# Kernel optimization log

Hardware: AMD Instinct MI355X
Metric: run time of the kernel (lower is better)

Reference implementation:

```python
import jax, jax.numpy as jnp
import numpy as np

N_NODES = 50000


def setup_inputs() -> dict:
    key = jax.random.key(0)
    ks = jax.random.split(key, 6)
    d_in, d_out = 256, 256
    n_edges = 1_600_000
    x = jax.random.normal(ks[0], (N_NODES, d_in), dtype=jnp.float32)
    edge_index = jax.random.randint(ks[1], (2, n_edges), 0, N_NODES, dtype=jnp.int64)
    edge_attr = jax.random.normal(ks[2], (n_edges, 16), dtype=jnp.float32)  # unused by forward
    W1 = jax.random.normal(ks[3], (d_in, d_out), dtype=jnp.float32) * (1.0 / np.sqrt(d_in))
    b1 = jnp.zeros((d_out,), dtype=jnp.float32)
    W2 = jax.random.normal(ks[4], (d_out, d_out), dtype=jnp.float32) * (1.0 / np.sqrt(d_out))
    b2 = jnp.zeros((d_out,), dtype=jnp.float32)
    eps = jnp.zeros((1,), dtype=jnp.float32)  # train_eps=True, init 0
    return {"x": x, "edge_index": edge_index, "edge_attr": edge_attr,
            "W1": W1, "b1": b1, "W2": W2, "b2": b2, "eps": eps}


def reference(x, edge_index, edge_attr, W1, b1, W2, b2, eps):
    src, dst = edge_index[0], edge_index[1]
    # sum aggregation: agg[i] = sum_{(j->i) in E} x[j]
    agg = jax.ops.segment_sum(x[src], dst, num_segments=N_NODES)  # [N, d_in]
    h = (1.0 + eps[0]) * x + agg
    # MLP: Linear -> ReLU -> (dropout=0) -> Linear
    h = jax.nn.relu(h @ W1 + b1)
    out = h @ W2 + b2
    return out
```

## Files before the change

kernel.cpp:

```cpp
#include <hip/hip_runtime.h>
#include <stdint.h>

#define NODES 50000
#define D 256
#define MP 50048
#define NBUCK 196
#define CAP 10240
#define EPB 4096
#define HS_LD 264

typedef short bf16x8 __attribute__((ext_vector_type(8)));
typedef float f32x4 __attribute__((ext_vector_type(4)));

__device__ inline unsigned short f2b(float f) {
    unsigned int u = __float_as_uint(f);
    unsigned int r = (u + 0x7fffu + ((u >> 16) & 1u)) >> 16;
    return (unsigned short)r;
}

__device__ inline bool ei_is64(const int* ei) {
    return (ei[1] | ei[3] | ei[5] | ei[7]) == 0;
}
__device__ inline int ei_get(const int* __restrict__ ei, long long pos, bool is64) {
    return is64 ? ei[2 * pos] : ei[(int)pos];
}

__global__ __launch_bounds__(256) void cast_x_kernel(const float* __restrict__ x,
                                                     unsigned short* __restrict__ xb,
                                                     int* __restrict__ bcnt) {
    if (blockIdx.x == 0 && threadIdx.x < NBUCK) bcnt[threadIdx.x] = 0;
    int t = blockIdx.x * 256 + threadIdx.x;
    float4 v = ((const float4*)x)[t];
    unsigned int lo = (unsigned int)f2b(v.x) | ((unsigned int)f2b(v.y) << 16);
    unsigned int hi = (unsigned int)f2b(v.z) | ((unsigned int)f2b(v.w) << 16);
    ((uint2*)xb)[t] = make_uint2(lo, hi);
}

__global__ __launch_bounds__(256) void pack_w_kernel(const float* __restrict__ W1,
                                                     const float* __restrict__ W2,
                                                     unsigned short* __restrict__ P1,
                                                     unsigned short* __restrict__ P2) {
    int t = blockIdx.x * 256 + threadIdx.x;
    const float* W = (t < 8192) ? W1 : W2;
    unsigned short* P = (t < 8192) ? P1 : P2;
    int u = t & 8191;
    int lane = u & 63, nt = (u >> 6) & 15, s = u >> 10;
    int q = lane >> 4, n = nt * 16 + (lane & 15);
    int kbase = s * 32 + q * 8;
#pragma unroll
    for (int j = 0; j < 8; j++) P[u * 8 + j] = f2b(W[(kbase + j) * D + n]);
}

__global__ __launch_bounds__(256) void partA_kernel(const int* __restrict__ ei, int E,
                                                    int* __restrict__ bcnt,
                                                    unsigned int* __restrict__ ebufT) {
    __shared__ int cnt[256];
    __shared__ int gbase[256];
    __shared__ int lcur[256];
    bool is64 = ei_is64(ei);
    int tid = threadIdx.x;
    cnt[tid] = 0;
    lcur[tid] = 0;
    __syncthreads();
    long long blockStart = (long long)blockIdx.x * EPB;
    unsigned int w[16];
    int bk[16];
#pragma unroll
    for (int r = 0; r < 16; r++) {
        long long e = blockStart + r * 256 + tid;
        bk[r] = -1;
        if (e < E) {
            int src = ei_get(ei, e, is64);
            int dst = ei_get(ei, (long long)E + e, is64);
            bk[r] = dst >> 8;
            w[r] = ((unsigned int)(dst & 255) << 16) | (unsigned int)src;
            atomicAdd(&cnt[bk[r]], 1);
        }
    }
    __syncthreads();
    if (tid < NBUCK && cnt[tid] > 0) gbase[tid] = atomicAdd(&bcnt[tid], cnt[tid]);
    __syncthreads();
#pragma unroll
    for (int r = 0; r < 16; r++) {
        if (bk[r] >= 0) {
            int p = atomicAdd(&lcur[bk[r]], 1);
            ebufT[(size_t)bk[r] * CAP + gbase[bk[r]] + p] = w[r];
        }
    }
}

__global__ __launch_bounds__(256) void bscan_kernel(const int* __restrict__ bcnt,
                                                    int* __restrict__ bstart,
                                                    int* __restrict__ offs, int E) {
    __shared__ int buf[256];
    int tid = threadIdx.x;
    int v = (tid < NBUCK) ? bcnt[tid] : 0;
    buf[tid] = v;
    __syncthreads();
    for (int off = 1; off < 256; off <<= 1) {
        int xv = (tid >= off) ? buf[tid - off] : 0;
        __syncthreads();
        buf[tid] += xv;
        __syncthreads();
    }
    if (tid < NBUCK) bstart[tid] = buf[tid] - v;
    if (tid == 0) offs[NODES] = E;
}

__global__ __launch_bounds__(256) void partB_kernel(const int* __restrict__ bcnt,
                                                    const int* __restrict__ bstart,
                                                    const unsigned int* __restrict__ ebufT,
                                                    int* __restrict__ offs,
                                                    int* __restrict__ ebuf) {
    __shared__ int ncnt[256];
    __shared__ int ncur[256];
    int b = blockIdx.x, tid = threadIdx.x;
    int n = bcnt[b];
    int base = bstart[b];
    ncnt[tid] = 0;
    __syncthreads();
    const unsigned int* reg = ebufT + (size_t)b * CAP;
    for (int i = tid; i < n; i += 256) {
        unsigned int w = reg[i];
        atomicAdd(&ncnt[w >> 16], 1);
    }
    __syncthreads();
    int v = ncnt[tid];
    ncur[tid] = v;
    __syncthreads();
    for (int off = 1; off < 256; off <<= 1) {
        int xv = (tid >= off) ? ncur[tid - off] : 0;
        __syncthreads();
        ncur[tid] += xv;
        __syncthreads();
    }
    int excl = ncur[tid] - v;
    int node = b * 256 + tid;
    if (node < NODES) offs[node] = base + excl;
    __syncthreads();
    ncur[tid] = excl;
    __syncthreads();
    for (int i = tid; i < n; i += 256) {
        unsigned int w = reg[i];
        int p = atomicAdd(&ncur[w >> 16], 1);
        ebuf[base + p] = (int)(w & 0xffffu);
    }
}

__device__ inline void upk_add(uint4 w, float* a) {
    a[0] += __uint_as_float(w.x << 16);
    a[1] += __uint_as_float(w.x & 0xffff0000u);
    a[2] += __uint_as_float(w.y << 16);
    a[3] += __uint_as_float(w.y & 0xffff0000u);
    a[4] += __uint_as_float(w.z << 16);
    a[5] += __uint_as_float(w.z & 0xffff0000u);
    a[6] += __uint_as_float(w.w << 16);
    a[7] += __uint_as_float(w.w & 0xffff0000u);
}

__global__ __launch_bounds__(256) void agg_kernel(const unsigned short* __restrict__ xb,
                                                  const int* __restrict__ offs,
                                                  const int* __restrict__ ebuf,
                                                  const float* __restrict__ eps,
                                                  unsigned short* __restrict__ h0) {
    int wv = (blockIdx.x * 256 + threadIdx.x) >> 6;
    int lane = threadIdx.x & 63;
    if (wv >= NODES) return;
    int half = lane >> 5;
    int l32 = lane & 31;
    float aA[8] = {0, 0, 0, 0, 0, 0, 0, 0};
    float aB[8] = {0, 0, 0, 0, 0, 0, 0, 0};
    int beg = offs[wv], end = offs[wv + 1];
    for (int base = beg; base < end; base += 64) {
        int id = 0;
        if (base + lane < end) id = ebuf[base + lane];
        int m = min(64, end - base);
        int j = 0;
        for (; j + 4 <= m; j += 4) {
            int sA = __shfl(id, j + half);
            int sB = __shfl(id, j + 2 + half);
            uint4 wA = *(const uint4*)(xb + (size_t)sA * D + l32 * 8);
            uint4 wB = *(const uint4*)(xb + (size_t)sB * D + l32 * 8);
            upk_add(wA, aA);
            upk_add(wB, aB);
        }
        for (; j + 2 <= m; j += 2) {
            int sA = __shfl(id, j + half);
            uint4 wA = *(const uint4*)(xb + (size_t)sA * D + l32 * 8);
            upk_add(wA, aA);
        }
        if (j < m) {
            int sA = __shfl(id, j);
            if (half == 0) {
                uint4 wA = *(const uint4*)(xb + (size_t)sA * D + l32 * 8);
                upk_add(wA, aA);
            }
        }
    }
    float a[8];
#pragma unroll
    for (int i = 0; i < 8; i++) {
        a[i] = aA[i] + aB[i];
        a[i] += __shfl_xor(a[i], 32);
    }
    if (half == 0) {
        float scale = 1.0f + eps[0];
        uint4 v = *(const uint4*)(xb + (size_t)wv * D + l32 * 8);
        a[0] += scale * __uint_as_float(v.x << 16);
        a[1] += scale * __uint_as_float(v.x & 0xffff0000u);
        a[2] += scale * __uint_as_float(v.y << 16);
        a[3] += scale * __uint_as_float(v.y & 0xffff0000u);
        a[4] += scale * __uint_as_float(v.z << 16);
        a[5] += scale * __uint_as_float(v.z & 0xffff0000u);
        a[6] += scale * __uint_as_float(v.w << 16);
        a[7] += scale * __uint_as_float(v.w & 0xffff0000u);
        uint4 o;
        o.x = (unsigned int)f2b(a[0]) | ((unsigned int)f2b(a[1]) << 16);
        o.y = (unsigned int)f2b(a[2]) | ((unsigned int)f2b(a[3]) << 16);
        o.z = (unsigned int)f2b(a[4]) | ((unsigned int)f2b(a[5]) << 16);
        o.w = (unsigned int)f2b(a[6]) | ((unsigned int)f2b(a[7]) << 16);
        ((uint4*)(h0 + (size_t)wv * D))[l32] = o;
    }
}

__global__ __launch_bounds__(256) void gemm_fused_kernel(const unsigned short* __restrict__ A,
                                                         const unsigned short* __restrict__ P1,
                                                         const float* __restrict__ b1,
                                                         const unsigned short* __restrict__ P2,
                                                         const float* __restrict__ b2,
                                                         float* __restrict__ out, int Mvalid) {
    __shared__ unsigned short hs[64 * HS_LD];
    int wv = threadIdx.x >> 6;
    int lane = threadIdx.x & 63;
    int quad = lane >> 4, l16 = lane & 15;
    int mBase = blockIdx.x * 64;
    const bf16x8* B1v = (const bf16x8*)P1;
    const bf16x8* B2v = (const bf16x8*)P2;

    {
        f32x4 acc[4][4] = {};
#pragma unroll
        for (int ks = 0; ks < 8; ks++) {
            bf16x8 af[4], bf[4];
#pragma unroll
            for (int mi = 0; mi < 4; mi++) {
                int row = mBase + mi * 16 + l16;
                af[mi] = *(const bf16x8*)(A + (size_t)row * D + ks * 32 + quad * 8);
            }
#pragma unroll
            for (int ni = 0; ni < 4; ni++) bf[ni] = B1v[(ks * 16 + wv * 4 + ni) * 64 + lane];
#pragma unroll
            for (int mi = 0; mi < 4; mi++)
#pragma unroll
                for (int ni = 0; ni < 4; ni++)
                    acc[mi][ni] = __builtin_amdgcn_mfma_f32_16x16x32_bf16(af[mi], bf[ni],
                                                                          acc[mi][ni], 0, 0, 0);
        }
#pragma unroll
        for (int mi = 0; mi < 4; mi++)
#pragma unroll
            for (int ni = 0; ni < 4; ni++) {
                int col = wv * 64 + ni * 16 + l16;
                float bs = b1[col];
#pragma unroll
                for (int r = 0; r < 4; r++) {
                    int rl = mi * 16 + quad * 4 + r;
                    hs[rl * HS_LD + col] = f2b(fmaxf(acc[mi][ni][r] + bs, 0.0f));
                }
            }
    }
    __syncthreads();

    f32x4 acc[4][4] = {};
#pragma unroll
    for (int ks = 0; ks < 8; ks++) {
        bf16x8 af[4], bf[4];
#pragma unroll
        for (int mi = 0; mi < 4; mi++)
            af[mi] = *(const bf16x8*)(hs + (mi * 16 + l16) * HS_LD + ks * 32 + quad * 8);
#pragma unroll
        for (int ni = 0; ni < 4; ni++) bf[ni] = B2v[(ks * 16 + wv * 4 + ni) * 64 + lane];
#pragma unroll
        for (int mi = 0; mi < 4; mi++)
#pragma unroll
            for (int ni = 0; ni < 4; ni++)
                acc[mi][ni] =
                    __builtin_amdgcn_mfma_f32_16x16x32_bf16(af[mi], bf[ni], acc[mi][ni], 0, 0, 0);
    }
#pragma unroll
    for (int mi = 0; mi < 4; mi++)
#pragma unroll
        for (int ni = 0; ni < 4; ni++) {
            int col = wv * 64 + ni * 16 + l16;
            float bs = b2[col];
#pragma unroll
            for (int r = 0; r < 4; r++) {
                int row = mBase + mi * 16 + quad * 4 + r;
                if (row < Mvalid) out[(size_t)row * D + col] = acc[mi][ni][r] + bs;
            }
        }
}

extern "C" void kernel_launch(void* const* d_in, const int* in_sizes, int n_in,
                              void* d_out, int out_size, void* d_ws, size_t ws_size,
                              hipStream_t stream) {
    const float* x = (const float*)d_in[0];
    const int* ei = (const int*)d_in[1];
    const float* W1 = (const float*)d_in[3];
    const float* b1 = (const float*)d_in[4];
    const float* W2 = (const float*)d_in[5];
    const float* b2 = (const float*)d_in[6];
    const float* eps = (const float*)d_in[7];
    int E = in_sizes[1] / 2;

    char* p = (char*)d_ws;
    auto alloc = [&](size_t bytes) {
        char* r = p;
        p += (bytes + 255) & ~(size_t)255;
        return r;
    };
    unsigned short* xb = (unsigned short*)alloc((size_t)MP * D * 2);
    unsigned short* h0 = (unsigned short*)alloc((size_t)MP * D * 2);
    unsigned short* P1 = (unsigned short*)alloc(8192 * 8 * 2);
    unsigned short* P2 = (unsigned short*)alloc(8192 * 8 * 2);
    int* bcnt = (int*)alloc((size_t)NBUCK * 4);
    int* bstart = (int*)alloc((size_t)(NBUCK + 1) * 4);
    int* offs = (int*)alloc((size_t)(NODES + 1) * 4);
    int* ebuf = (int*)alloc((size_t)E * 4);
    unsigned int* ebufT = (unsigned int*)alloc((size_t)NBUCK * CAP * 4);

    cast_x_kernel<<<NODES * D / 4 / 256, 256, 0, stream>>>(x, xb, bcnt);
    pack_w_kernel<<<64, 256, 0, stream>>>(W1, W2, P1, P2);
    partA_kernel<<<(E + EPB - 1) / EPB, 256, 0, stream>>>(ei, E, bcnt, ebufT);
    bscan_kernel<<<1, 256, 0, stream>>>(bcnt, bstart, offs, E);
    partB_kernel<<<NBUCK, 256, 0, stream>>>(bcnt, bstart, ebufT, offs, ebuf);
    agg_kernel<<<(NODES + 3) / 4, 256, 0, stream>>>(xb, offs, ebuf, eps, h0);
    gemm_fused_kernel<<<MP / 64, 256, 0, stream>>>(h0, P1, b1, P2, b2, (float*)d_out, NODES);
}
```

Measured before the change: 379.7 us.

## Fuse prep kernels, vectorize edge loads, widen partB, simplify gather loop

Merges the x cast and weight packing into one launch. partA now loads two edges per thread with vector loads. partB uses 1024 threads per bucket block so the histogram and scatter loops have more parallelism. The aggregation loop drops the per-64-edge shuffle broadcast, reads indices straight from ebuf and issues four row gathers per iteration, trading shuffle overhead for redundant index loads.

```diff
diff --git a/kernel.cpp b/kernel.cpp
--- a/kernel.cpp
+++ b/kernel.cpp
@@ -8,6 +8,7 @@
 #define CAP 10240
 #define EPB 4096
 #define HS_LD 264
+#define CAST_BLOCKS 12500
 
 typedef short bf16x8 __attribute__((ext_vector_type(8)));
 typedef float f32x4 __attribute__((ext_vector_type(4)));
@@ -25,30 +26,32 @@
     return is64 ? ei[2 * pos] : ei[(int)pos];
 }
 
-__global__ __launch_bounds__(256) void cast_x_kernel(const float* __restrict__ x,
-                                                     unsigned short* __restrict__ xb,
-                                                     int* __restrict__ bcnt) {
-    if (blockIdx.x == 0 && threadIdx.x < NBUCK) bcnt[threadIdx.x] = 0;
-    int t = blockIdx.x * 256 + threadIdx.x;
-    float4 v = ((const float4*)x)[t];
-    unsigned int lo = (unsigned int)f2b(v.x) | ((unsigned int)f2b(v.y) << 16);
-    unsigned int hi = (unsigned int)f2b(v.z) | ((unsigned int)f2b(v.w) << 16);
-    ((uint2*)xb)[t] = make_uint2(lo, hi);
-}
-
-__global__ __launch_bounds__(256) void pack_w_kernel(const float* __restrict__ W1,
-                                                     const float* __restrict__ W2,
-                                                     unsigned short* __restrict__ P1,
-                                                     unsigned short* __restrict__ P2) {
-    int t = blockIdx.x * 256 + threadIdx.x;
-    const float* W = (t < 8192) ? W1 : W2;
-    unsigned short* P = (t < 8192) ? P1 : P2;
-    int u = t & 8191;
-    int lane = u & 63, nt = (u >> 6) & 15, s = u >> 10;
-    int q = lane >> 4, n = nt * 16 + (lane & 15);
-    int kbase = s * 32 + q * 8;
-#pragma unroll
-    for (int j = 0; j < 8; j++) P[u * 8 + j] = f2b(W[(kbase + j) * D + n]);
+__global__ __launch_bounds__(256) void prep_kernel(const float* __restrict__ x,
+                                                   unsigned short* __restrict__ xb,
+                                                   int* __restrict__ bcnt,
+                                                   const float* __restrict__ W1,
+                                                   const float* __restrict__ W2,
+                                                   unsigned short* __restrict__ P1,
+                                                   unsigned short* __restrict__ P2) {
+    int blk = blockIdx.x;
+    if (blk < CAST_BLOCKS) {
+        if (blk == 0 && threadIdx.x < NBUCK) bcnt[threadIdx.x] = 0;
+        int t = blk * 256 + threadIdx.x;
+        float4 v = ((const float4*)x)[t];
+        unsigned int lo = (unsigned int)f2b(v.x) | ((unsigned int)f2b(v.y) << 16);
+        unsigned int hi = (unsigned int)f2b(v.z) | ((unsigned int)f2b(v.w) << 16);
+        ((uint2*)xb)[t] = make_uint2(lo, hi);
+    } else {
+        int t = (blk - CAST_BLOCKS) * 256 + threadIdx.x;
+        const float* W = (t < 8192) ? W1 : W2;
+        unsigned short* P = (t < 8192) ? P1 : P2;
+        int u = t & 8191;
+        int lane = u & 63, nt = (u >> 6) & 15, s = u >> 10;
+        int q = lane >> 4, n = nt * 16 + (lane & 15);
+        int kbase = s * 32 + q * 8;
+#pragma unroll
+        for (int j = 0; j < 8; j++) P[u * 8 + j] = f2b(W[(kbase + j) * D + n]);
+    }
 }
 
 __global__ __launch_bounds__(256) void partA_kernel(const int* __restrict__ ei, int E,
@@ -62,20 +65,35 @@
     cnt[tid] = 0;
     lcur[tid] = 0;
     __syncthreads();
-    long long blockStart = (long long)blockIdx.x * EPB;
+    long long pairBase = ((long long)blockIdx.x * EPB) >> 1;
     unsigned int w[16];
     int bk[16];
 #pragma unroll
-    for (int r = 0; r < 16; r++) {
-        long long e = blockStart + r * 256 + tid;
-        bk[r] = -1;
-        if (e < E) {
-            int src = ei_get(ei, e, is64);
-            int dst = ei_get(ei, (long long)E + e, is64);
-            bk[r] = dst >> 8;
-            w[r] = ((unsigned int)(dst & 255) << 16) | (unsigned int)src;
-            atomicAdd(&cnt[bk[r]], 1);
+    for (int r = 0; r < 8; r++) {
+        long long pp = pairBase + (long long)r * 256 + tid;
+        long long e0 = pp * 2;
+        int s0 = 0, s1 = 0, d0 = 0, d1 = 0;
+        bool v1 = (e0 + 1 < E), v0 = (e0 < E);
+        if (v1) {
+            if (is64) {
+                uint4 sv = *(const uint4*)(ei + 4 * pp);
+                uint4 dv = *(const uint4*)(ei + (size_t)2 * E + 4 * pp);
+                s0 = (int)sv.x; s1 = (int)sv.z; d0 = (int)dv.x; d1 = (int)dv.z;
+            } else {
+                uint2 sv = *(const uint2*)(ei + 2 * pp);
+                uint2 dv = *(const uint2*)(ei + (size_t)E + 2 * pp);
+                s0 = (int)sv.x; s1 = (int)sv.y; d0 = (int)dv.x; d1 = (int)dv.y;
+            }
+        } else if (v0) {
+            s0 = ei_get(ei, e0, is64);
+            d0 = ei_get(ei, (long long)E + e0, is64);
         }
+        bk[2 * r] = v0 ? (d0 >> 8) : -1;
+        bk[2 * r + 1] = v1 ? (d1 >> 8) : -1;
+        w[2 * r] = ((unsigned int)(d0 & 255) << 16) | (unsigned int)s0;
+        w[2 * r + 1] = ((unsigned int)(d1 & 255) << 16) | (unsigned int)s1;
+        if (v0) atomicAdd(&cnt[bk[2 * r]], 1);
+        if (v1) atomicAdd(&cnt[bk[2 * r + 1]], 1);
     }
     __syncthreads();
     if (tid < NBUCK && cnt[tid] > 0) gbase[tid] = atomicAdd(&bcnt[tid], cnt[tid]);
@@ -107,40 +125,42 @@
     if (tid == 0) offs[NODES] = E;
 }
 
-__global__ __launch_bounds__(256) void partB_kernel(const int* __restrict__ bcnt,
-                                                    const int* __restrict__ bstart,
-                                                    const unsigned int* __restrict__ ebufT,
-                                                    int* __restrict__ offs,
-                                                    int* __restrict__ ebuf) {
+__global__ __launch_bounds__(1024) void partB_kernel(const int* __restrict__ bcnt,
+                                                     const int* __restrict__ bstart,
+                                                     const unsigned int* __restrict__ ebufT,
+                                                     int* __restrict__ offs,
+                                                     int* __restrict__ ebuf) {
     __shared__ int ncnt[256];
     __shared__ int ncur[256];
     int b = blockIdx.x, tid = threadIdx.x;
     int n = bcnt[b];
     int base = bstart[b];
-    ncnt[tid] = 0;
+    if (tid < 256) ncnt[tid] = 0;
     __syncthreads();
     const unsigned int* reg = ebufT + (size_t)b * CAP;
-    for (int i = tid; i < n; i += 256) {
-        unsigned int w = reg[i];
-        atomicAdd(&ncnt[w >> 16], 1);
-    }
-    __syncthreads();
-    int v = ncnt[tid];
-    ncur[tid] = v;
+    for (int i = tid; i < n; i += 1024) atomicAdd(&ncnt[reg[i] >> 16], 1);
+    __syncthreads();
+    int v = 0;
+    if (tid < 256) {
+        v = ncnt[tid];
+        ncur[tid] = v;
+    }
     __syncthreads();
     for (int off = 1; off < 256; off <<= 1) {
-        int xv = (tid >= off) ? ncur[tid - off] : 0;
+        int xv = 0;
+        if (tid < 256 && tid >= off) xv = ncur[tid - off];
         __syncthreads();
-        ncur[tid] += xv;
+        if (tid < 256) ncur[tid] += xv;
         __syncthreads();
     }
-    int excl = ncur[tid] - v;
-    int node = b * 256 + tid;
-    if (node < NODES) offs[node] = base + excl;
-    __syncthreads();
-    ncur[tid] = excl;
-    __syncthreads();
-    for (int i = tid; i < n; i += 256) {
+    if (tid < 256) {
+        int excl = ncur[tid] - v;
+        int node = b * 256 + tid;
+        if (node < NODES) offs[node] = base + excl;
+        ncur[tid] = excl;
+    }
+    __syncthreads();
+    for (int i = tid; i < n; i += 1024) {
         unsigned int w = reg[i];
         int p = atomicAdd(&ncur[w >> 16], 1);
         ebuf[base + p] = (int)(w & 0xffffu);
@@ -171,31 +191,30 @@
     float aA[8] = {0, 0, 0, 0, 0, 0, 0, 0};
     float aB[8] = {0, 0, 0, 0, 0, 0, 0, 0};
     int beg = offs[wv], end = offs[wv + 1];
-    for (int base = beg; base < end; base += 64) {
-        int id = 0;
-        if (base + lane < end) id = ebuf[base + lane];
-        int m = min(64, end - base);
-        int j = 0;
-        for (; j + 4 <= m; j += 4) {
-            int sA = __shfl(id, j + half);
-            int sB = __shfl(id, j + 2 + half);
-            uint4 wA = *(const uint4*)(xb + (size_t)sA * D + l32 * 8);
-            uint4 wB = *(const uint4*)(xb + (size_t)sB * D + l32 * 8);
-            upk_add(wA, aA);
-            upk_add(wB, aB);
-        }
-        for (; j + 2 <= m; j += 2) {
-            int sA = __shfl(id, j + half);
-            uint4 wA = *(const uint4*)(xb + (size_t)sA * D + l32 * 8);
-            upk_add(wA, aA);
-        }
-        if (j < m) {
-            int sA = __shfl(id, j);
-            if (half == 0) {
-                uint4 wA = *(const uint4*)(xb + (size_t)sA * D + l32 * 8);
-                upk_add(wA, aA);
-            }
-        }
+    int j = beg;
+    for (; j + 8 <= end; j += 8) {
+        int i0 = ebuf[j + half];
+        int i1 = ebuf[j + 2 + half];
+        int i2 = ebuf[j + 4 + half];
+        int i3 = ebuf[j + 6 + half];
+        uint4 w0 = *(const uint4*)(xb + (size_t)i0 * D + l32 * 8);
+        uint4 w1 = *(const uint4*)(xb + (size_t)i1 * D + l32 * 8);
+        uint4 w2 = *(const uint4*)(xb + (size_t)i2 * D + l32 * 8);
+        uint4 w3 = *(const uint4*)(xb + (size_t)i3 * D + l32 * 8);
+        upk_add(w0, aA);
+        upk_add(w1, aB);
+        upk_add(w2, aA);
+        upk_add(w3, aB);
+    }
+    for (; j + 2 <= end; j += 2) {
+        int i0 = ebuf[j + half];
+        uint4 w0 = *(const uint4*)(xb + (size_t)i0 * D + l32 * 8);
+        upk_add(w0, aA);
+    }
+    if (j < end && half == 0) {
+        int i0 = ebuf[j];
+        uint4 w0 = *(const uint4*)(xb + (size_t)i0 * D + l32 * 8);
+        upk_add(w0, aA);
     }
     float a[8];
 #pragma unroll
@@ -329,11 +348,10 @@
     int* ebuf = (int*)alloc((size_t)E * 4);
     unsigned int* ebufT = (unsigned int*)alloc((size_t)NBUCK * CAP * 4);
 
-    cast_x_kernel<<<NODES * D / 4 / 256, 256, 0, stream>>>(x, xb, bcnt);
-    pack_w_kernel<<<64, 256, 0, stream>>>(W1, W2, P1, P2);
+    prep_kernel<<<CAST_BLOCKS + 64, 256, 0, stream>>>(x, xb, bcnt, W1, W2, P1, P2);
     partA_kernel<<<(E + EPB - 1) / EPB, 256, 0, stream>>>(ei, E, bcnt, ebufT);
     bscan_kernel<<<1, 256, 0, stream>>>(bcnt, bstart, offs, E);
-    partB_kernel<<<NBUCK, 256, 0, stream>>>(bcnt, bstart, ebufT, offs, ebuf);
+    partB_kernel<<<NBUCK, 1024, 0, stream>>>(bcnt, bstart, ebufT, offs, ebuf);
     agg_kernel<<<(NODES + 3) / 4, 256, 0, stream>>>(xb, offs, ebuf, eps, h0);
     gemm_fused_kernel<<<MP / 64, 256, 0, stream>>>(h0, P1, b1, P2, b2, (float*)d_out, NODES);
 }
```

Result: faster. 364.4 us (-4.0%).
